# Optimization experiments

Measured on AMD Instinct MI355X. Metric: run time of the kernel, lower is better.

Reference implementation:

```python
import jax, jax.numpy as jnp
import numpy as np

B, S, D = 2, 2048, 1024
H = 16
HD = D // H  # 64
SCALE = HD ** 0.5


def setup_inputs() -> dict:
    key = jax.random.key(0)
    ks = jax.random.split(key, 9)
    std = 1.0 / np.sqrt(D)
    inp = {"x": jax.random.normal(ks[0], (B, S, D), dtype=jnp.float32)}
    names = ["Wq", "Wk", "Wv", "Wo"]
    for i, n in enumerate(names):
        inp[n] = jax.random.uniform(ks[1 + i], (D, D), dtype=jnp.float32, minval=-std, maxval=std)
        inp["b" + n[1]] = jax.random.uniform(ks[5 + i], (D,), dtype=jnp.float32, minval=-std, maxval=std)
    return inp


def reference(x, Wq, Wk, Wv, Wo, bq, bk, bv, bo):
    # QKV projections (torch Linear: y = x @ W.T + b; here W stored as [in, out] already transposed)
    q = x @ Wq + bq
    k = x @ Wk + bk
    v = x @ Wv + bv
    # [B, H, S, HD]
    q = q.reshape(B, S, H, HD).transpose(0, 2, 1, 3)
    k = k.reshape(B, S, H, HD).transpose(0, 2, 1, 3)
    v = v.reshape(B, S, H, HD).transpose(0, 2, 1, 3)
    scores = jnp.einsum("bhqd,bhkd->bhqk", q, k) / SCALE  # [B, H, S, S]
    causal = jnp.tril(jnp.ones((S, S), dtype=bool))
    scores = jnp.where(causal, scores, -jnp.inf)
    attn = jax.nn.softmax(scores, axis=-1)  # dropout p=0.0 (eval)
    ctx = jnp.einsum("bhqk,bhkd->bhqd", attn, v)
    ctx = ctx.transpose(0, 2, 1, 3).reshape(B, S, D)
    return ctx @ Wo + bo
```

## Files before the change

kernel.cpp:

```cpp
#include <hip/hip_runtime.h>


#define S_LEN 2048
#define DMODEL 1024
#define NHEAD 16
#define HDIM 64
#define MROWS 4096

typedef __bf16 bf16x8 __attribute__((ext_vector_type(8)));
typedef float f32x4 __attribute__((ext_vector_type(4)));
typedef float f32x16 __attribute__((ext_vector_type(16)));

__device__ __forceinline__ ushort f2bf(float f) {
  union { float f; unsigned u; } v; v.f = f;
  unsigned r = v.u + 0x7fffu + ((v.u >> 16) & 1u);
  return (ushort)(r >> 16);
}

__device__ __forceinline__ void gload_lds16(const ushort* g, ushort* l) {
  __builtin_amdgcn_global_load_lds(
      (const __attribute__((address_space(1))) void*)g,
      (__attribute__((address_space(3))) void*)l, 16, 0, 0);
}

__device__ __forceinline__ unsigned pack2bf(float lo, float hi) {
  union { __bf16 h[2]; unsigned u; } t;
  t.h[0] = (__bf16)lo; t.h[1] = (__bf16)hi;
  return t.u;
}

#if __has_builtin(__builtin_amdgcn_permlane32_swap)
#define HAVE_PL32 1
__device__ __forceinline__ void pl32sw(unsigned& a, unsigned& b) {
  auto r = __builtin_amdgcn_permlane32_swap((int)a, (int)b, false, false);
  a = (unsigned)r[0];
  b = (unsigned)r[1];
}
#endif

__device__ __forceinline__ float halfcomb_max(float x) {
#ifdef HAVE_PL32
  unsigned a = __float_as_uint(x), b = a;
  pl32sw(a, b);
  return fmaxf(__uint_as_float(a), __uint_as_float(b));
#else
  return fmaxf(x, __shfl_xor(x, 32, 64));
#endif
}
__device__ __forceinline__ float halfcomb_sum(float x) {
#ifdef HAVE_PL32
  unsigned a = __float_as_uint(x), b = a;
  pl32sw(a, b);
  return __uint_as_float(a) + __uint_as_float(b);
#else
  return x + __shfl_xor(x, 32, 64);
#endif
}


__global__ __launch_bounds__(256) void cvt_x(const float* __restrict__ x,
                                             ushort* __restrict__ xb) {
  int i = (blockIdx.x * 256 + threadIdx.x) * 4;
  float4 v = *(const float4*)&x[i];
  ushort4 o;
  o.x = f2bf(v.x); o.y = f2bf(v.y); o.z = f2bf(v.z); o.w = f2bf(v.w);
  *(ushort4*)&xb[i] = o;
}

__global__ __launch_bounds__(256) void cvt_wt(const float* __restrict__ W0,
                                              const float* __restrict__ W1,
                                              const float* __restrict__ W2,
                                              const float* __restrict__ W3,
                                              ushort* __restrict__ out) {
  const float* W = blockIdx.z == 0 ? W0 : blockIdx.z == 1 ? W1
                   : blockIdx.z == 2 ? W2 : W3;
  ushort* WT = out + (size_t)blockIdx.z * DMODEL * DMODEL;
  __shared__ float tile[64][65];
  const int n0 = blockIdx.x * 64, k0 = blockIdx.y * 64;
#pragma unroll
  for (int i = 0; i < 4; ++i) {
    int chunk = i * 256 + threadIdx.x;
    int r = chunk >> 4, c4 = chunk & 15;
    float4 v = *(const float4*)&W[(size_t)(k0 + r) * DMODEL + n0 + c4 * 4];
    tile[r][c4 * 4 + 0] = v.x; tile[r][c4 * 4 + 1] = v.y;
    tile[r][c4 * 4 + 2] = v.z; tile[r][c4 * 4 + 3] = v.w;
  }
  __syncthreads();
#pragma unroll
  for (int i = 0; i < 4; ++i) {
    int chunk = i * 256 + threadIdx.x;
    int r = chunk >> 4, c4 = chunk & 15;
    ushort4 o;
    o.x = f2bf(tile[c4 * 4 + 0][r]); o.y = f2bf(tile[c4 * 4 + 1][r]);
    o.z = f2bf(tile[c4 * 4 + 2][r]); o.w = f2bf(tile[c4 * 4 + 3][r]);
    *(ushort4*)&WT[(size_t)(n0 + r) * DMODEL + k0 + c4 * 4] = o;
  }
}

__global__ __launch_bounds__(256) void trV(const ushort* __restrict__ V,
                                           ushort* __restrict__ Vt) {
  const int bh = blockIdx.z;
  const ushort* src = V + (size_t)bh * S_LEN * HDIM;
  ushort* dst = Vt + (size_t)bh * HDIM * S_LEN;
  __shared__ ushort tile[32][33];
  int s0 = blockIdx.x * 32, h0 = blockIdx.y * 32;
  int tx = threadIdx.x & 31, ty = threadIdx.x >> 5;
#pragma unroll
  for (int i = 0; i < 32; i += 8)
    tile[ty + i][tx] = src[(size_t)(s0 + ty + i) * HDIM + h0 + tx];
  __syncthreads();
#pragma unroll
  for (int i = 0; i < 32; i += 8)
    dst[(size_t)(h0 + ty + i) * S_LEN + s0 + tx] = tile[tx][ty + i];
}

__global__ __launch_bounds__(512) void gemm256(
    const ushort* __restrict__ A, const ushort* __restrict__ Bt,
    const float* __restrict__ b0, const float* __restrict__ b1,
    const float* __restrict__ b2, ushort* __restrict__ outQ,
    ushort* __restrict__ outK, ushort* __restrict__ outV) {
  const int flat = blockIdx.y * 16 + blockIdx.x;
  const int swz = (flat & 7) * 32 + (flat >> 3);
  const int bx = swz & 15, by = swz >> 4;
  const int m0 = bx * 256, n0 = by * 192;

  __shared__ __align__(16) ushort Al[2][256 * 64];
  __shared__ __align__(16) ushort Bl[2][192 * 64];

  const int tid = threadIdx.x;
  const int lane = tid & 63, wid = tid >> 6;
  const int wr = wid >> 2, wc = wid & 3;
  const int fr = lane & 15, hi16 = lane >> 4;

  f32x4 acc[8][3] = {};

#pragma unroll
  for (int l = 0; l < 4; ++l) {
    int chunk = l * 512 + tid;
    int row = chunk >> 3, cpos = chunk & 7;
    int scol = (cpos ^ (row & 7)) * 8;
    gload_lds16(&A[(size_t)(m0 + row) * DMODEL + scol], &Al[0][chunk * 8]);
  }
#pragma unroll
  for (int l = 0; l < 3; ++l) {
    int chunk = l * 512 + tid;
    int row = chunk >> 3, cpos = chunk & 7;
    int scol = (cpos ^ (row & 7)) * 8;
    gload_lds16(&Bt[(size_t)(n0 + row) * DMODEL + scol], &Bl[0][chunk * 8]);
  }
  __syncthreads();

  for (int t = 0; t < 16; ++t) {
    const int bt = t & 1;
    bf16x8 bfr[3];
#pragma unroll
    for (int s = 0; s < 4; ++s) {
      const int kk = s >> 1, mh = s & 1;
      bf16x8 af[4];
#pragma unroll
      for (int q = 0; q < 4; ++q) {
        int rl = wr * 128 + (mh * 4 + q) * 16 + fr;
        af[q] = *(const bf16x8*)&Al[bt][rl * 64 +
                                        ((kk * 4 + hi16) ^ (rl & 7)) * 8];
      }
      if (mh == 0) {
#pragma unroll
        for (int nf = 0; nf < 3; ++nf) {
          int rl = wc * 48 + nf * 16 + fr;
          bfr[nf] = *(const bf16x8*)&Bl[bt][rl * 64 +
                                            ((kk * 4 + hi16) ^ (rl & 7)) * 8];
        }
      }
      if (t + 1 < 16 && s < 2) {
        const int k64 = (t + 1) * 64;
        if (s == 0) {
#pragma unroll
          for (int l = 0; l < 4; ++l) {
            int chunk = l * 512 + tid;
            int row = chunk >> 3, cpos = chunk & 7;
            int scol = (cpos ^ (row & 7)) * 8;
            gload_lds16(&A[(size_t)(m0 + row) * DMODEL + k64 + scol],
                        &Al[bt ^ 1][chunk * 8]);
          }
        } else {
#pragma unroll
          for (int l = 0; l < 3; ++l) {
            int chunk = l * 512 + tid;
            int row = chunk >> 3, cpos = chunk & 7;
            int scol = (cpos ^ (row & 7)) * 8;
            gload_lds16(&Bt[(size_t)(n0 + row) * DMODEL + k64 + scol],
                        &Bl[bt ^ 1][chunk * 8]);
          }
        }
      }
      __builtin_amdgcn_s_barrier();
      __builtin_amdgcn_s_setprio(1);
#pragma unroll
      for (int q = 0; q < 4; ++q)
#pragma unroll
        for (int nf = 0; nf < 3; ++nf)
          acc[mh * 4 + q][nf] = __builtin_amdgcn_mfma_f32_16x16x32_bf16(
              af[q], bfr[nf], acc[mh * 4 + q][nf], 0, 0, 0);
      __builtin_amdgcn_s_setprio(0);
      if (s < 3) __builtin_amdgcn_s_barrier();
    }
    __syncthreads();
  }

#pragma unroll
  for (int mf = 0; mf < 8; ++mf) {
#pragma unroll
    for (int nf = 0; nf < 3; ++nf) {
      int col = n0 + wc * 48 + nf * 16 + fr;
      int z = col >> 10, cw = col & 1023;
      float bval = z == 0 ? b0[cw] : z == 1 ? b1[cw] : b2[cw];
      int h = cw >> 6, hd = cw & (HDIM - 1);
      ushort* dst = (z == 0) ? outQ : (z == 1) ? outK : outV;
#pragma unroll
      for (int rg = 0; rg < 4; ++rg) {
        int row = m0 + wr * 128 + mf * 16 + hi16 * 4 + rg;
        int b = row >> 11, sq = row & (S_LEN - 1);
        float val = acc[mf][nf][rg] + bval;
        dst[(((size_t)(b * NHEAD + h)) * S_LEN + sq) * HDIM + hd] = f2bf(val);
      }
    }
  }
}

__global__ __launch_bounds__(256) void gemm128o(
    const ushort* __restrict__ A, const ushort* __restrict__ Bt,
    const float* __restrict__ b0, float* __restrict__ outB) {
  const int NT = 256;
  const int flat = blockIdx.y * 32 + blockIdx.x;
  const int swz = (flat & 7) * (NT >> 3) + (flat >> 3);
  const int bx = swz & 31, by = swz >> 5;
  const int m0 = bx * 128, n0 = by * 128;

  __shared__ __align__(16) ushort Alds[2][128 * 64];
  __shared__ __align__(16) ushort Blds[2][128 * 64];

  const int tid = threadIdx.x;
  const int lane = tid & 63, w = tid >> 6;
  const int wr = w >> 1, wc = w & 1;
  const int fr = lane & 15, hi16 = lane >> 4;

  f32x4 acc[4][4] = {};

#pragma unroll
  for (int it = 0; it < 4; ++it) {
    int c = it * 256 + tid;
    int row = c >> 3;
    int sc = ((c & 7) ^ (row & 7)) * 8;
    gload_lds16(&A[(size_t)(m0 + row) * DMODEL + sc], &Alds[0][c * 8]);
    gload_lds16(&Bt[(size_t)(n0 + row) * DMODEL + sc], &Blds[0][c * 8]);
  }
  __syncthreads();

  for (int t = 0; t < 16; ++t) {
    const int bt = t & 1;
#pragma unroll
    for (int s = 0; s < 2; ++s) {
      bf16x8 af[4], bfr[4];
#pragma unroll
      for (int i = 0; i < 4; ++i) {
        int row = wr * 64 + i * 16 + fr;
        af[i] = *(const bf16x8*)&Alds[bt][row * 64 +
                                          ((s * 4 + hi16) ^ (row & 7)) * 8];
      }
#pragma unroll
      for (int j = 0; j < 4; ++j) {
        int row = wc * 64 + j * 16 + fr;
        bfr[j] = *(const bf16x8*)&Blds[bt][row * 64 +
                                           ((s * 4 + hi16) ^ (row & 7)) * 8];
      }
      if (t + 1 < 16) {
        const int k64 = (t + 1) * 64;
#pragma unroll
        for (int it = 0; it < 4; ++it) {
          int c = it * 256 + tid;
          int row = c >> 3;
          int sc = ((c & 7) ^ (row & 7)) * 8;
          if (s == 0)
            gload_lds16(&A[(size_t)(m0 + row) * DMODEL + k64 + sc],
                        &Alds[bt ^ 1][c * 8]);
          else
            gload_lds16(&Bt[(size_t)(n0 + row) * DMODEL + k64 + sc],
                        &Blds[bt ^ 1][c * 8]);
        }
      }
      __builtin_amdgcn_s_barrier();
      __builtin_amdgcn_s_setprio(1);
#pragma unroll
      for (int i = 0; i < 4; ++i)
#pragma unroll
        for (int j = 0; j < 4; ++j)
          acc[i][j] = __builtin_amdgcn_mfma_f32_16x16x32_bf16(af[i], bfr[j],
                                                              acc[i][j], 0, 0, 0);
      __builtin_amdgcn_s_setprio(0);
      if (s < 1) __builtin_amdgcn_s_barrier();
    }
    __syncthreads();
  }

#pragma unroll
  for (int i = 0; i < 4; ++i) {
#pragma unroll
    for (int j = 0; j < 4; ++j) {
      int col = n0 + wc * 64 + j * 16 + fr;
      float bval = b0[col];
#pragma unroll
      for (int r = 0; r < 4; ++r) {
        int row = m0 + wr * 64 + i * 16 + hi16 * 4 + r;
        outB[(size_t)row * DMODEL + col] = acc[i][j][r] + bval;
      }
    }
  }
}

__global__ __launch_bounds__(256, 2) void attn4(const ushort* __restrict__ Q,
                                                const ushort* __restrict__ K,
                                                const ushort* __restrict__ Vt,
                                                ushort* __restrict__ ctx) {
  const int n = blockIdx.x;
  const int v = (n & 7) * 64 + (n >> 3);
  const int ptile = v & 15, bh = v >> 4;
  const int b = bh >> 4, h = bh & 15;
  const int tid = threadIdx.x;
  const int lane = tid & 63, wid = tid >> 6;
  const int p = wid >> 1;
  const int wq = wid & 1;
  const int q32 = lane & 31, hi = lane >> 5;
  const bool lo_half = (hi == 0);
  const int tid2 = tid & 127;

  const ushort* Qb = Q + (size_t)bh * S_LEN * HDIM;
  const ushort* Kb = K + (size_t)bh * S_LEN * HDIM;
  const ushort* Vb = Vt + (size_t)bh * HDIM * S_LEN;

  __shared__ __align__(16) ushort Kl[2][2][64 * 64];
  __shared__ __align__(16) ushort Vl[2][2][64 * 64];
  float* scr = (float*)&Kl[0][0][0];

  const float C = 0.125f * 1.44269504f;

  for (int ph = 0; ph < 2; ++ph) {
    const int j = ph ? 31 - ptile : ptile;
    const int qbase = j * 64 + wq * 32;
    const int qrow = qbase + q32;

    bf16x8 qf[4];
#pragma unroll
    for (int s = 0; s < 4; ++s)
      qf[s] = *(const bf16x8*)&Qb[(size_t)qrow * HDIM + s * 16 + hi * 8];

    f32x16 oaccA[2] = {}, oaccB[2] = {};
    float mraw = -1e30f, lsum = 0.f;
    const int NS = (j >> 1) + 1;

    if (p <= j) {
      const int kv = p * 64;
#pragma unroll
      for (int it = 0; it < 4; ++it) {
        int chunk = it * 128 + tid2;
        int row = chunk >> 3, sc = ((chunk & 7) ^ (row & 7)) * 8;
        gload_lds16(&Kb[(size_t)(kv + row) * HDIM + sc], &Kl[p][0][chunk * 8]);
        gload_lds16(&Vb[(size_t)row * S_LEN + kv + sc], &Vl[p][0][chunk * 8]);
      }
    }
    __syncthreads();

    int buf = 0;
    for (int it = 0; it < NS; ++it) {
      const int s = 2 * it + p;
      const int kv0 = s * 64;

      if (s + 2 <= j) {
        const int kvn = kv0 + 128;
#pragma unroll
        for (int st = 0; st < 4; ++st) {
          int chunk = st * 128 + tid2;
          int row = chunk >> 3, sc = ((chunk & 7) ^ (row & 7)) * 8;
          gload_lds16(&Kb[(size_t)(kvn + row) * HDIM + sc],
                      &Kl[p][buf ^ 1][chunk * 8]);
          gload_lds16(&Vb[(size_t)row * S_LEN + kvn + sc],
                      &Vl[p][buf ^ 1][chunk * 8]);
        }
      }

      if (s <= j) {
        const int rsw = (q32 & 7);
        f32x16 sa[2] = {};
        __builtin_amdgcn_s_setprio(1);
#pragma unroll
        for (int sl = 0; sl < 4; ++sl) {
          bf16x8 kf0 = *(const bf16x8*)&Kl[p][buf][q32 * 64 +
                                                   ((sl * 2 + hi) ^ rsw) * 8];
          bf16x8 kf1 = *(const bf16x8*)&Kl[p][buf][(32 + q32) * 64 +
                                                   ((sl * 2 + hi) ^ rsw) * 8];
          sa[0] = __builtin_amdgcn_mfma_f32_32x32x16_bf16(kf0, qf[sl], sa[0],
                                                          0, 0, 0);
          sa[1] = __builtin_amdgcn_mfma_f32_32x32x16_bf16(kf1, qf[sl], sa[1],
                                                          0, 0, 0);
        }
        __builtin_amdgcn_s_setprio(0);

        bf16x8 vf[2][4];
#pragma unroll
        for (int t2 = 0; t2 < 2; ++t2) {
          const int row = t2 * 32 + q32;
#pragma unroll
          for (int sl = 0; sl < 4; ++sl)
            vf[t2][sl] = *(const bf16x8*)&Vl[p][buf][row * 64 +
                                                     ((sl * 2 + hi) ^ rsw) * 8];
        }

        if (kv0 + 63 > qbase) {
          const int khi = kv0 + 4 * hi;
#pragma unroll
          for (int t = 0; t < 2; ++t)
#pragma unroll
            for (int rr = 0; rr < 16; ++rr) {
              int kg = khi + t * 32 + (rr & 3) + 8 * (rr >> 2);
              if (kg > qrow) sa[t][rr] = -1e30f;
            }
        }

        float tmv[8];
#pragma unroll
        for (int rr = 0; rr < 8; ++rr)
          tmv[rr] = fmaxf(fmaxf(sa[0][rr], sa[0][rr + 8]),
                          fmaxf(sa[1][rr], sa[1][rr + 8]));
        float t0 = fmaxf(fmaxf(tmv[0], tmv[1]), fmaxf(tmv[2], tmv[3]));
        float t1 = fmaxf(fmaxf(tmv[4], tmv[5]), fmaxf(tmv[6], tmv[7]));
        float tm = halfcomb_max(fmaxf(t0, t1));

        if (!__all(tm <= mraw + 64.f)) {
          float mnew = fmaxf(mraw, tm);
          float alpha = __builtin_exp2f((mraw - mnew) * C);
          lsum *= alpha;
#pragma unroll
          for (int rr = 0; rr < 16; ++rr) {
            oaccA[0][rr] *= alpha; oaccA[1][rr] *= alpha;
            oaccB[0][rr] *= alpha; oaccB[1][rr] *= alpha;
          }
          mraw = mnew;
        }
        const float mC = mraw * C;
        float psum = 0.f;
#pragma unroll
        for (int t = 0; t < 2; ++t)
#pragma unroll
          for (int rr = 0; rr < 16; ++rr) {
            float pp = __builtin_exp2f(__builtin_fmaf(sa[t][rr], C, -mC));
            sa[t][rr] = pp;
            psum += pp;
          }
        lsum += halfcomb_sum(psum);

        __builtin_amdgcn_s_setprio(1);
#pragma unroll
        for (int t = 0; t < 2; ++t) {
#pragma unroll
          for (int half = 0; half < 2; ++half) {
            const int rb = half * 8;
            unsigned a0 = pack2bf(sa[t][rb + 0], sa[t][rb + 1]);
            unsigned a1 = pack2bf(sa[t][rb + 2], sa[t][rb + 3]);
            unsigned b0w = pack2bf(sa[t][rb + 4], sa[t][rb + 5]);
            unsigned b1w = pack2bf(sa[t][rb + 6], sa[t][rb + 7]);
            union { unsigned u[4]; bf16x8 v; } pf;
#ifdef HAVE_PL32
            pl32sw(a0, b0w);
            pl32sw(a1, b1w);
            pf.u[0] = a0; pf.u[1] = a1; pf.u[2] = b0w; pf.u[3] = b1w;
#else
            unsigned xa0 = __shfl_xor(a0, 32, 64);
            unsigned xa1 = __shfl_xor(a1, 32, 64);
            unsigned xb0 = __shfl_xor(b0w, 32, 64);
            unsigned xb1 = __shfl_xor(b1w, 32, 64);
            pf.u[0] = lo_half ? a0 : xb0;
            pf.u[1] = lo_half ? a1 : xb1;
            pf.u[2] = lo_half ? xa0 : b0w;
            pf.u[3] = lo_half ? xa1 : b1w;
#endif
            if (t == 0) {
              oaccA[0] = __builtin_amdgcn_mfma_f32_32x32x16_bf16(
                  vf[0][half], pf.v, oaccA[0], 0, 0, 0);
              oaccA[1] = __builtin_amdgcn_mfma_f32_32x32x16_bf16(
                  vf[1][half], pf.v, oaccA[1], 0, 0, 0);
            } else {
              oaccB[0] = __builtin_amdgcn_mfma_f32_32x32x16_bf16(
                  vf[0][2 + half], pf.v, oaccB[0], 0, 0, 0);
              oaccB[1] = __builtin_amdgcn_mfma_f32_32x32x16_bf16(
                  vf[1][2 + half], pf.v, oaccB[1], 0, 0, 0);
            }
          }
        }
        __builtin_amdgcn_s_setprio(0);
      }

      __syncthreads();
      buf ^= 1;
    }

#pragma unroll
    for (int tt = 0; tt < 2; ++tt)
#pragma unroll
      for (int rr = 0; rr < 16; ++rr) oaccA[tt][rr] += oaccB[tt][rr];

    const int base = (wq * 64 + lane) * 37;
    if (p == 1) {
      scr[base + 0] = mraw;
      scr[base + 1] = lsum;
#pragma unroll
      for (int t = 0; t < 2; ++t)
#pragma unroll
        for (int rr = 0; rr < 16; ++rr)
          scr[base + 2 + t * 16 + rr] = oaccA[t][rr];
    }
    __syncthreads();
    if (p == 0) {
      const float mB = scr[base + 0], lB = scr[base + 1];
      const float mS = fmaxf(mraw, mB);
      const float aA = __builtin_exp2f((mraw - mS) * C);
      const float aB = __builtin_exp2f((mB - mS) * C);
      const float lT = lsum * aA + lB * aB;
      const float linv = 1.0f / lT;
      ushort* crow = &ctx[((size_t)(b * S_LEN) + qrow) * DMODEL + h * HDIM];
#pragma unroll
      for (int t = 0; t < 2; ++t)
#pragma unroll
        for (int g2 = 0; g2 < 4; ++g2) {
          ushort4 o;
          float m0 = oaccA[t][g2 * 4 + 0] * aA + scr[base + 2 + t * 16 + g2 * 4 + 0] * aB;
          float m1 = oaccA[t][g2 * 4 + 1] * aA + scr[base + 2 + t * 16 + g2 * 4 + 1] * aB;
          float m2 = oaccA[t][g2 * 4 + 2] * aA + scr[base + 2 + t * 16 + g2 * 4 + 2] * aB;
          float m3 = oaccA[t][g2 * 4 + 3] * aA + scr[base + 2 + t * 16 + g2 * 4 + 3] * aB;
          o.x = f2bf(m0 * linv); o.y = f2bf(m1 * linv);
          o.z = f2bf(m2 * linv); o.w = f2bf(m3 * linv);
          *(ushort4*)&crow[t * 32 + g2 * 8 + hi * 4] = o;
        }
    }
    __syncthreads();
  }
}


extern "C" void kernel_launch(void* const* d_in, const int* in_sizes, int n_in,
                              void* d_out, int out_size, void* d_ws,
                              size_t ws_size, hipStream_t stream) {
  const float* x  = (const float*)d_in[0];
  const float* Wq = (const float*)d_in[1];
  const float* bq = (const float*)d_in[2];
  const float* Wk = (const float*)d_in[3];
  const float* bk = (const float*)d_in[4];
  const float* Wv = (const float*)d_in[5];
  const float* bv = (const float*)d_in[6];
  const float* Wo = (const float*)d_in[7];
  const float* bo = (const float*)d_in[8];

  char* ws = (char*)d_ws;
  ushort* Xbf = (ushort*)ws;
  ushort* WT  = (ushort*)(ws + (size_t)8 * 1024 * 1024);
  ushort* QKV = (ushort*)(ws + (size_t)16 * 1024 * 1024);
  ushort* CTX = (ushort*)(ws + (size_t)40 * 1024 * 1024);

  const size_t QKV_ELEMS = (size_t)MROWS * DMODEL;
  const size_t W_ELEMS = (size_t)DMODEL * DMODEL;

  ushort* Qp  = QKV;
  ushort* Kp  = QKV + QKV_ELEMS;
  ushort* Vtp = QKV + 2 * QKV_ELEMS;
  ushort* Vrp = CTX;

  cvt_x<<<4096, 256, 0, stream>>>(x, Xbf);
  cvt_wt<<<dim3(16, 16, 4), 256, 0, stream>>>(Wq, Wk, Wv, Wo, WT);
  gemm256<<<dim3(16, 16), 512, 0, stream>>>(Xbf, WT, bq, bk, bv, Qp, Kp, Vrp);
  trV<<<dim3(64, 2, 32), 256, 0, stream>>>(Vrp, Vtp);
  attn4<<<dim3(512), 256, 0, stream>>>(Qp, Kp, Vtp, CTX);
  gemm128o<<<dim3(32, 8), 256, 0, stream>>>(CTX, WT + 3 * W_ELEMS, bo,
                                            (float*)d_out);
}
```

Baseline: 119.8 us.

## Widen attention blocks to 128 query rows with 8 waves sharing KV tiles

```diff
diff --git a/kernel.cpp b/kernel.cpp
--- a/kernel.cpp
+++ b/kernel.cpp
@@ -317,36 +317,38 @@
   }
 }
 
-__global__ __launch_bounds__(256, 2) void attn4(const ushort* __restrict__ Q,
+__global__ __launch_bounds__(512, 1) void attn8(const ushort* __restrict__ Q,
                                                 const ushort* __restrict__ K,
                                                 const ushort* __restrict__ Vt,
                                                 ushort* __restrict__ ctx) {
-  const int n = blockIdx.x;
-  const int v = (n & 7) * 64 + (n >> 3);
-  const int ptile = v & 15, bh = v >> 4;
+  const int blk = blockIdx.x;
+  const int w2 = (blk & 7) * 32 + (blk >> 3);
+  const int bh = w2 >> 3, ptile = w2 & 7;
   const int b = bh >> 4, h = bh & 15;
   const int tid = threadIdx.x;
   const int lane = tid & 63, wid = tid >> 6;
-  const int p = wid >> 1;
-  const int wq = wid & 1;
+  const int p = wid >> 2;
+  const int wq = wid & 3;
   const int q32 = lane & 31, hi = lane >> 5;
   const bool lo_half = (hi == 0);
-  const int tid2 = tid & 127;
+  const int tidp = tid & 255;
 
   const ushort* Qb = Q + (size_t)bh * S_LEN * HDIM;
   const ushort* Kb = K + (size_t)bh * S_LEN * HDIM;
   const ushort* Vb = Vt + (size_t)bh * HDIM * S_LEN;
 
-  __shared__ __align__(16) ushort Kl[2][2][64 * 64];
-  __shared__ __align__(16) ushort Vl[2][2][64 * 64];
-  float* scr = (float*)&Kl[0][0][0];
+  __shared__ __align__(16) ushort lds[32768];
+  ushort* Klp = lds;
+  ushort* Vlp = lds + 16384;
+  float* scr = (float*)lds;
 
   const float C = 0.125f * 1.44269504f;
 
   for (int ph = 0; ph < 2; ++ph) {
-    const int j = ph ? 31 - ptile : ptile;
-    const int qbase = j * 64 + wq * 32;
+    const int T = ph ? 15 - ptile : ptile;
+    const int qbase = T * 128 + wq * 32;
     const int qrow = qbase + q32;
+    const int NS = T + 1;
 
     bf16x8 qf[4];
 #pragma unroll
@@ -355,16 +357,17 @@
 
     f32x16 oaccA[2] = {}, oaccB[2] = {};
     float mraw = -1e30f, lsum = 0.f;
-    const int NS = (j >> 1) + 1;
-
-    if (p <= j) {
+
+    {
       const int kv = p * 64;
 #pragma unroll
-      for (int it = 0; it < 4; ++it) {
-        int chunk = it * 128 + tid2;
+      for (int g = 0; g < 2; ++g) {
+        int chunk = g * 256 + tidp;
         int row = chunk >> 3, sc = ((chunk & 7) ^ (row & 7)) * 8;
-        gload_lds16(&Kb[(size_t)(kv + row) * HDIM + sc], &Kl[p][0][chunk * 8]);
-        gload_lds16(&Vb[(size_t)row * S_LEN + kv + sc], &Vl[p][0][chunk * 8]);
+        gload_lds16(&Kb[(size_t)(kv + row) * HDIM + sc],
+                    &Klp[(p * 2 + 0) * 4096 + chunk * 8]);
+        gload_lds16(&Vb[(size_t)row * S_LEN + kv + sc],
+                    &Vlp[(p * 2 + 0) * 4096 + chunk * 8]);
       }
     }
     __syncthreads();
@@ -374,29 +377,31 @@
       const int s = 2 * it + p;
       const int kv0 = s * 64;
 
-      if (s + 2 <= j) {
+      if (it + 1 < NS) {
         const int kvn = kv0 + 128;
 #pragma unroll
-        for (int st = 0; st < 4; ++st) {
-          int chunk = st * 128 + tid2;
+        for (int g = 0; g < 2; ++g) {
+          int chunk = g * 256 + tidp;
           int row = chunk >> 3, sc = ((chunk & 7) ^ (row & 7)) * 8;
           gload_lds16(&Kb[(size_t)(kvn + row) * HDIM + sc],
-                      &Kl[p][buf ^ 1][chunk * 8]);
+                      &Klp[(p * 2 + (buf ^ 1)) * 4096 + chunk * 8]);
           gload_lds16(&Vb[(size_t)row * S_LEN + kvn + sc],
-                      &Vl[p][buf ^ 1][chunk * 8]);
-        }
-      }
-
-      if (s <= j) {
+                      &Vlp[(p * 2 + (buf ^ 1)) * 4096 + chunk * 8]);
+        }
+      }
+
+      if (kv0 <= qbase + 31) {
+        const ushort* Kt = &Klp[(p * 2 + buf) * 4096];
+        const ushort* Vtl = &Vlp[(p * 2 + buf) * 4096];
         const int rsw = (q32 & 7);
+
         f32x16 sa[2] = {};
         __builtin_amdgcn_s_setprio(1);
 #pragma unroll
         for (int sl = 0; sl < 4; ++sl) {
-          bf16x8 kf0 = *(const bf16x8*)&Kl[p][buf][q32 * 64 +
-                                                   ((sl * 2 + hi) ^ rsw) * 8];
-          bf16x8 kf1 = *(const bf16x8*)&Kl[p][buf][(32 + q32) * 64 +
-                                                   ((sl * 2 + hi) ^ rsw) * 8];
+          bf16x8 kf0 = *(const bf16x8*)&Kt[q32 * 64 + ((sl * 2 + hi) ^ rsw) * 8];
+          bf16x8 kf1 = *(const bf16x8*)&Kt[(32 + q32) * 64 +
+                                           ((sl * 2 + hi) ^ rsw) * 8];
           sa[0] = __builtin_amdgcn_mfma_f32_32x32x16_bf16(kf0, qf[sl], sa[0],
                                                           0, 0, 0);
           sa[1] = __builtin_amdgcn_mfma_f32_32x32x16_bf16(kf1, qf[sl], sa[1],
@@ -410,8 +415,8 @@
           const int row = t2 * 32 + q32;
 #pragma unroll
           for (int sl = 0; sl < 4; ++sl)
-            vf[t2][sl] = *(const bf16x8*)&Vl[p][buf][row * 64 +
-                                                     ((sl * 2 + hi) ^ rsw) * 8];
+            vf[t2][sl] = *(const bf16x8*)&Vtl[row * 64 +
+                                              ((sl * 2 + hi) ^ rsw) * 8];
         }
 
         if (kv0 + 63 > qbase) {
@@ -576,7 +581,7 @@
   cvt_wt<<<dim3(16, 16, 4), 256, 0, stream>>>(Wq, Wk, Wv, Wo, WT);
   gemm256<<<dim3(16, 16), 512, 0, stream>>>(Xbf, WT, bq, bk, bv, Qp, Kp, Vrp);
   trV<<<dim3(64, 2, 32), 256, 0, stream>>>(Vrp, Vtp);
-  attn4<<<dim3(512), 256, 0, stream>>>(Qp, Kp, Vtp, CTX);
+  attn8<<<dim3(256), 512, 0, stream>>>(Qp, Kp, Vtp, CTX);
   gemm128o<<<dim3(32, 8), 256, 0, stream>>>(CTX, WT + 3 * W_ELEMS, bo,
                                             (float*)d_out);
 }
```

New measurement: 118.2 us. No clear change (-1.3%).
